# Kernel optimization log

Measured on AMD Instinct MI355X. Metric: run time of the kernel, lower is better.

## Reference

```python
import jax, jax.numpy as jnp
import numpy as np

N = 50000      # nodes
E = 800000     # edges (before self loops)
IN_DIM = 128
HID = 16
HEADS = 8
OUT_DIM = 40
NEG_SLOPE = 0.2


def setup_inputs() -> dict:
    key = jax.random.key(0)
    ks = jax.random.split(key, 10)
    x = jax.random.normal(ks[0], (N, IN_DIM), jnp.float32)
    edge_index = jax.random.randint(ks[1], (2, E), 0, N, dtype=jnp.int32)
    # layer 1: GATConv(IN_DIM, HID, heads=HEADS, concat=True)
    W1 = jax.random.normal(ks[2], (IN_DIM, HEADS * HID), jnp.float32) / np.sqrt(IN_DIM).astype(np.float32)
    att_src1 = jax.random.normal(ks[3], (HEADS, HID), jnp.float32) * 0.1
    att_dst1 = jax.random.normal(ks[4], (HEADS, HID), jnp.float32) * 0.1
    bias1 = jnp.zeros((HEADS * HID,), jnp.float32)
    # layer 2: GATConv(HEADS*HID, OUT_DIM, heads=1, concat=False)
    W2 = jax.random.normal(ks[5], (HEADS * HID, OUT_DIM), jnp.float32) / np.sqrt(HEADS * HID).astype(np.float32)
    att_src2 = jax.random.normal(ks[6], (1, OUT_DIM), jnp.float32) * 0.1
    att_dst2 = jax.random.normal(ks[7], (1, OUT_DIM), jnp.float32) * 0.1
    bias2 = jnp.zeros((OUT_DIM,), jnp.float32)
    return {"x": x, "W1": W1, "att_src1": att_src1, "att_dst1": att_dst1, "bias1": bias1,
            "W2": W2, "att_src2": att_src2, "att_dst2": att_dst2, "bias2": bias2,
            "edge_index": edge_index}


def gat_conv(x, src, dst, W, att_src, att_dst, bias, heads, dim, concat, num_nodes):
    # h: [N, H, D]
    h = (x @ W).reshape(num_nodes, heads, dim)
    a_src = jnp.sum(h * att_src, axis=-1)  # [N, H]
    a_dst = jnp.sum(h * att_dst, axis=-1)  # [N, H]
    e = a_src[src] + a_dst[dst]            # [E', H]
    e = jnp.where(e > 0, e, NEG_SLOPE * e)  # leaky_relu
    # segment softmax over edges sharing the same target node
    m = jax.ops.segment_max(e, dst, num_segments=num_nodes)  # [N, H]
    e = jnp.exp(e - m[dst])
    s = jax.ops.segment_sum(e, dst, num_segments=num_nodes)  # [N, H]
    alpha = e / (s[dst] + 1e-16)            # [E', H]
    msg = h[src] * alpha[:, :, None]        # [E', H, D]
    out = jax.ops.segment_sum(msg, dst, num_segments=num_nodes)  # [N, H, D]
    if concat:
        out = out.reshape(num_nodes, heads * dim)
    else:
        out = out.mean(axis=1)
    return out + bias


def reference(x, W1, att_src1, att_dst1, bias1, W2, att_src2, att_dst2, bias2, edge_index):
    # add self loops (PyG GATConv default)
    loop = jnp.arange(N, dtype=edge_index.dtype)
    src = jnp.concatenate([edge_index[0], loop])
    dst = jnp.concatenate([edge_index[1], loop])
    # eval mode: dropout (p=0.6) is identity
    h = gat_conv(x, src, dst, W1, att_src1, att_dst1, bias1, HEADS, HID, True, N)
    h = jax.nn.elu(h)
    out = gat_conv(h, src, dst, W2, att_src2, att_dst2, bias2, 1, OUT_DIM, False, N)
    return jax.nn.log_softmax(out, axis=1)
```

## Files before the change

### kernel.cpp

```cpp
#include <hip/hip_runtime.h>
#include <math.h>

#define IN_DIM 128
#define HEADS 8
#define HID 16
#define OUT_DIM 40
#define NEG 0.2f
#define NSLICE 8

typedef short bf16x8 __attribute__((ext_vector_type(8)));
typedef float f32x4 __attribute__((ext_vector_type(4)));

__device__ __forceinline__ unsigned short f32_to_bf16_rne(float v) {
  unsigned u = __float_as_uint(v);
  return (unsigned short)((u + 0x7FFFu + ((u >> 16) & 1u)) >> 16);
}


__global__ void hist_k(const int* __restrict__ ei, int E0, int N, int snode,
                       int* __restrict__ deg) {
  int b = blockIdx.x;
  int slice = b & (NSLICE - 1);
  int e = (b >> 3) * 256 + threadIdx.x;
  int EP = E0 + N;
  if (e >= EP) return;
  int d = (e < E0) ? ei[E0 + e] : (e - E0);
  if (d / snode == slice) atomicAdd(&deg[d], 1);
}

__global__ __launch_bounds__(1024) void scanA_k(const int* __restrict__ deg, int* __restrict__ rp,
                                                int* __restrict__ bsum, int n) {
  __shared__ int wsum[16];
  int tid = threadIdx.x;
  int i = blockIdx.x * 1024 + tid;
  int lane = tid & 63, w = tid >> 6;
  int v = (i < n) ? deg[i] : 0;
  int x = v;
  #pragma unroll
  for (int off = 1; off < 64; off <<= 1) {
    int y = __shfl_up(x, off);
    if (lane >= off) x += y;
  }
  if (lane == 63) wsum[w] = x;
  __syncthreads();
  if (tid < 16) {
    int s = wsum[tid];
    #pragma unroll
    for (int off = 1; off < 16; off <<= 1) {
      int y = __shfl_up(s, off);
      if (tid >= off) s += y;
    }
    wsum[tid] = s;
  }
  __syncthreads();
  int woff = (w == 0) ? 0 : wsum[w - 1];
  if (i < n) rp[i] = woff + x - v;
  if (tid == 0) bsum[blockIdx.x] = wsum[15];
}

__global__ __launch_bounds__(1024) void scanB_k(int* __restrict__ bsum, int nb,
                                                int* __restrict__ rp, int n) {
  __shared__ int wsum[16];
  int tid = threadIdx.x;
  int lane = tid & 63, w = tid >> 6;
  int v = (tid < nb) ? bsum[tid] : 0;
  int x = v;
  #pragma unroll
  for (int off = 1; off < 64; off <<= 1) {
    int y = __shfl_up(x, off);
    if (lane >= off) x += y;
  }
  if (lane == 63) wsum[w] = x;
  __syncthreads();
  if (tid < 16) {
    int s = wsum[tid];
    #pragma unroll
    for (int off = 1; off < 16; off <<= 1) {
      int y = __shfl_up(s, off);
      if (tid >= off) s += y;
    }
    wsum[tid] = s;
  }
  __syncthreads();
  int woff = (w == 0) ? 0 : wsum[w - 1];
  if (tid < nb) bsum[tid] = woff + x - v;
  if (tid == 0) rp[n] = wsum[15];
}

__global__ __launch_bounds__(1024) void scanC_k(int* __restrict__ rp, const int* __restrict__ bsum,
                                                int* __restrict__ cnt, int n) {
  int i = blockIdx.x * 1024 + threadIdx.x;
  if (i < n) {
    int v = rp[i] + bsum[blockIdx.x];
    rp[i] = v;
    cnt[i] = v;
  }
}

__global__ void scatter_k(const int* __restrict__ ei, int E0, int N, int snode,
                          int* __restrict__ cnt, int* __restrict__ csr_src) {
  int b = blockIdx.x;
  int slice = b & (NSLICE - 1);
  int e = (b >> 3) * 256 + threadIdx.x;
  int EP = E0 + N;
  if (e >= EP) return;
  int d = (e < E0) ? ei[E0 + e] : (e - E0);
  if (d / snode != slice) return;
  int s = (e < E0) ? ei[e] : d;
  int pos = atomicAdd(&cnt[d], 1);
  csr_src[pos] = s;
}

__global__ void prep_k(const float* __restrict__ W1, const float* __restrict__ as1,
                       const float* __restrict__ ad1, const float* __restrict__ W2,
                       const float* __restrict__ as2, const float* __restrict__ ad2,
                       unsigned short* __restrict__ whi, unsigned short* __restrict__ wlo,
                       unsigned short* __restrict__ w2p, int* __restrict__ deg, int N) {
  int t = blockIdx.x * 256 + threadIdx.x;
  if (t < N) deg[t] = 0;
  if (t < 18432) {
    int j = t & 7, lane = (t >> 3) & 63, kc = (t >> 9) & 3, ct = t >> 11;
    int k = kc * 32 + (lane >> 4) * 8 + j;
    int col = lane & 15;
    float v;
    if (ct < 8) {
      v = W1[k * 128 + ct * 16 + col];
    } else {
      int h = col & 7;
      const float* att = (col < 8) ? as1 : ad1;
      float s = 0.f;
      #pragma unroll
      for (int d = 0; d < 16; ++d) s += W1[k * 128 + h * 16 + d] * att[h * 16 + d];
      v = s;
    }
    unsigned u = __float_as_uint(v);
    unsigned hi = (u + 0x7FFFu + ((u >> 16) & 1u)) >> 16;
    float rem = v - __uint_as_float(hi << 16);
    unsigned ur = __float_as_uint(rem);
    unsigned lo = (ur + 0x7FFFu + ((ur >> 16) & 1u)) >> 16;
    whi[t] = (unsigned short)hi;
    wlo[t] = (unsigned short)lo;
  } else if (t < 18432 + 6144) {
    int u2 = t - 18432;
    int j = u2 & 7, lane = (u2 >> 3) & 63, kc = (u2 >> 9) & 3, ct = u2 >> 11;
    int k = kc * 32 + (lane >> 4) * 8 + j;
    int col = ct * 16 + (lane & 15);
    float v;
    if (col < OUT_DIM) {
      v = W2[k * OUT_DIM + col];
    } else if (col < 42) {
      const float* att = (col == OUT_DIM) ? as2 : ad2;
      float s = 0.f;
      #pragma unroll 8
      for (int d = 0; d < OUT_DIM; ++d) s += W2[k * OUT_DIM + d] * att[d];
      v = s;
    } else {
      v = 0.f;
    }
    w2p[u2] = f32_to_bf16_rne(v);
  }
}

__global__ __launch_bounds__(256) void gemm1_mfma_k(
    const float* __restrict__ x, const unsigned short* __restrict__ whi,
    const unsigned short* __restrict__ wlo,
    unsigned short* __restrict__ h1, float* __restrict__ a1s, float* __restrict__ a1d, int N) {
  int w = threadIdx.x >> 6, lane = threadIdx.x & 63;
  int quad = lane >> 4, l15 = lane & 15;
  int row = blockIdx.x * 64 + w * 16 + l15;
  int rowc = (row < N) ? row : (N - 1);

  f32x4 acc[9];
  #pragma unroll
  for (int t = 0; t < 9; ++t) acc[t] = (f32x4){0.f, 0.f, 0.f, 0.f};

  const float* xr = x + (size_t)rowc * 128 + quad * 8;
  #pragma unroll
  for (int kc = 0; kc < 4; ++kc) {
    f32x4 a0 = *reinterpret_cast<const f32x4*>(xr + kc * 32);
    f32x4 a1 = *reinterpret_cast<const f32x4*>(xr + kc * 32 + 4);
    float av[8] = {a0.x, a0.y, a0.z, a0.w, a1.x, a1.y, a1.z, a1.w};
    bf16x8 ahi, alo;
    #pragma unroll
    for (int j = 0; j < 8; ++j) {
      unsigned u = __float_as_uint(av[j]);
      unsigned hi = (u + 0x7FFFu + ((u >> 16) & 1u)) >> 16;
      float rem = av[j] - __uint_as_float(hi << 16);
      unsigned ur = __float_as_uint(rem);
      unsigned lo = (ur + 0x7FFFu + ((ur >> 16) & 1u)) >> 16;
      ahi[j] = (short)hi;
      alo[j] = (short)lo;
    }
    #pragma unroll
    for (int ct = 0; ct < 9; ++ct) {
      bf16x8 bh = *reinterpret_cast<const bf16x8*>(whi + ((size_t)(ct * 4 + kc) * 64 + lane) * 8);
      bf16x8 bl = *reinterpret_cast<const bf16x8*>(wlo + ((size_t)(ct * 4 + kc) * 64 + lane) * 8);
      acc[ct] = __builtin_amdgcn_mfma_f32_16x16x32_bf16(ahi, bh, acc[ct], 0, 0, 0);
      acc[ct] = __builtin_amdgcn_mfma_f32_16x16x32_bf16(ahi, bl, acc[ct], 0, 0, 0);
      acc[ct] = __builtin_amdgcn_mfma_f32_16x16x32_bf16(alo, bh, acc[ct], 0, 0, 0);
    }
  }
  int rbase = blockIdx.x * 64 + w * 16 + quad * 4;
  #pragma unroll
  for (int reg = 0; reg < 4; ++reg) {
    int r = rbase + reg;
    if (r < N) {
      #pragma unroll
      for (int ct = 0; ct < 8; ++ct)
        h1[(size_t)r * 128 + ct * 16 + l15] = f32_to_bf16_rne(acc[ct][reg]);
      float v = acc[8][reg];
      if (l15 < 8) a1s[r * 8 + l15] = v;
      else         a1d[r * 8 + (l15 - 8)] = v;
    }
  }
}

__global__ __launch_bounds__(256) void agg1_k(
    const int* __restrict__ row_ptr, const int* __restrict__ csr_src,
    const float* __restrict__ a1s, const float* __restrict__ a1d,
    const unsigned* __restrict__ h1u, const float* __restrict__ bias1,
    unsigned* __restrict__ vrowp, int N) {
  int wid = threadIdx.x >> 6;
  int lane = threadIdx.x & 63;
  int n = blockIdx.x * 4 + wid;
  if (n >= N) return;

  int rs = row_ptr[n], re = row_ptr[n + 1];
  int h = lane >> 3;
  float adn = a1d[n * 8 + h];

  float accx = 0.f, accy = 0.f, sw = 0.f;
  int i = rs;
  for (; i + 8 <= re; i += 8) {
    int s0 = csr_src[i],     s1 = csr_src[i + 1], s2 = csr_src[i + 2], s3 = csr_src[i + 3];
    int s4 = csr_src[i + 4], s5 = csr_src[i + 5], s6 = csr_src[i + 6], s7 = csr_src[i + 7];
    float e0 = a1s[s0 * 8 + h] + adn;
    float e1 = a1s[s1 * 8 + h] + adn;
    float e2 = a1s[s2 * 8 + h] + adn;
    float e3 = a1s[s3 * 8 + h] + adn;
    float e4 = a1s[s4 * 8 + h] + adn;
    float e5 = a1s[s5 * 8 + h] + adn;
    float e6 = a1s[s6 * 8 + h] + adn;
    float e7 = a1s[s7 * 8 + h] + adn;
    unsigned u0 = h1u[(size_t)s0 * 64 + lane];
    unsigned u1 = h1u[(size_t)s1 * 64 + lane];
    unsigned u2 = h1u[(size_t)s2 * 64 + lane];
    unsigned u3 = h1u[(size_t)s3 * 64 + lane];
    unsigned u4 = h1u[(size_t)s4 * 64 + lane];
    unsigned u5 = h1u[(size_t)s5 * 64 + lane];
    unsigned u6 = h1u[(size_t)s6 * 64 + lane];
    unsigned u7 = h1u[(size_t)s7 * 64 + lane];
    e0 = fmaxf(e0, NEG * e0); e1 = fmaxf(e1, NEG * e1);
    e2 = fmaxf(e2, NEG * e2); e3 = fmaxf(e3, NEG * e3);
    e4 = fmaxf(e4, NEG * e4); e5 = fmaxf(e5, NEG * e5);
    e6 = fmaxf(e6, NEG * e6); e7 = fmaxf(e7, NEG * e7);
    float w0 = __expf(e0), w1 = __expf(e1), w2 = __expf(e2), w3 = __expf(e3);
    float w4 = __expf(e4), w5 = __expf(e5), w6 = __expf(e6), w7 = __expf(e7);
    sw += ((w0 + w1) + (w2 + w3)) + ((w4 + w5) + (w6 + w7));
    accx += w0 * __uint_as_float(u0 << 16) + w1 * __uint_as_float(u1 << 16)
          + w2 * __uint_as_float(u2 << 16) + w3 * __uint_as_float(u3 << 16)
          + w4 * __uint_as_float(u4 << 16) + w5 * __uint_as_float(u5 << 16)
          + w6 * __uint_as_float(u6 << 16) + w7 * __uint_as_float(u7 << 16);
    accy += w0 * __uint_as_float(u0 & 0xFFFF0000u) + w1 * __uint_as_float(u1 & 0xFFFF0000u)
          + w2 * __uint_as_float(u2 & 0xFFFF0000u) + w3 * __uint_as_float(u3 & 0xFFFF0000u)
          + w4 * __uint_as_float(u4 & 0xFFFF0000u) + w5 * __uint_as_float(u5 & 0xFFFF0000u)
          + w6 * __uint_as_float(u6 & 0xFFFF0000u) + w7 * __uint_as_float(u7 & 0xFFFF0000u);
  }
  for (; i + 4 <= re; i += 4) {
    int s0 = csr_src[i], s1 = csr_src[i + 1], s2 = csr_src[i + 2], s3 = csr_src[i + 3];
    float e0 = a1s[s0 * 8 + h] + adn;
    float e1 = a1s[s1 * 8 + h] + adn;
    float e2 = a1s[s2 * 8 + h] + adn;
    float e3 = a1s[s3 * 8 + h] + adn;
    unsigned u0 = h1u[(size_t)s0 * 64 + lane];
    unsigned u1 = h1u[(size_t)s1 * 64 + lane];
    unsigned u2 = h1u[(size_t)s2 * 64 + lane];
    unsigned u3 = h1u[(size_t)s3 * 64 + lane];
    e0 = fmaxf(e0, NEG * e0); e1 = fmaxf(e1, NEG * e1);
    e2 = fmaxf(e2, NEG * e2); e3 = fmaxf(e3, NEG * e3);
    float w0 = __expf(e0), w1 = __expf(e1), w2 = __expf(e2), w3 = __expf(e3);
    sw += (w0 + w1) + (w2 + w3);
    accx += w0 * __uint_as_float(u0 << 16) + w1 * __uint_as_float(u1 << 16)
          + w2 * __uint_as_float(u2 << 16) + w3 * __uint_as_float(u3 << 16);
    accy += w0 * __uint_as_float(u0 & 0xFFFF0000u) + w1 * __uint_as_float(u1 & 0xFFFF0000u)
          + w2 * __uint_as_float(u2 & 0xFFFF0000u) + w3 * __uint_as_float(u3 & 0xFFFF0000u);
  }
  for (; i < re; ++i) {
    int s = csr_src[i];
    float e = a1s[s * 8 + h] + adn;
    e = fmaxf(e, NEG * e);
    float w = __expf(e);
    unsigned u = h1u[(size_t)s * 64 + lane];
    sw += w;
    accx += w * __uint_as_float(u << 16);
    accy += w * __uint_as_float(u & 0xFFFF0000u);
  }
  float inv = 1.f / (sw + 1e-16f);
  float2 b = *reinterpret_cast<const float2*>(bias1 + 2 * lane);
  float vx = accx * inv + b.x;
  float vy = accy * inv + b.y;
  vx = (vx > 0.f) ? vx : (__expf(vx) - 1.f);
  vy = (vy > 0.f) ? vy : (__expf(vy) - 1.f);
  unsigned packed = (unsigned)f32_to_bf16_rne(vx) | ((unsigned)f32_to_bf16_rne(vy) << 16);
  vrowp[(size_t)n * 64 + lane] = packed;
}

__global__ __launch_bounds__(256) void gemm2_mfma_k(
    const unsigned short* __restrict__ vrow, const unsigned short* __restrict__ w2p,
    unsigned short* __restrict__ h2, float* __restrict__ a2s, float* __restrict__ a2d, int N) {
  int w = threadIdx.x >> 6, lane = threadIdx.x & 63;
  int quad = lane >> 4, l15 = lane & 15;
  int row = blockIdx.x * 64 + w * 16 + l15;
  int rowc = (row < N) ? row : (N - 1);

  f32x4 acc[3];
  #pragma unroll
  for (int t = 0; t < 3; ++t) acc[t] = (f32x4){0.f, 0.f, 0.f, 0.f};

  const unsigned short* vr = vrow + (size_t)rowc * 128 + quad * 8;
  #pragma unroll
  for (int kc = 0; kc < 4; ++kc) {
    bf16x8 a = *reinterpret_cast<const bf16x8*>(vr + kc * 32);
    #pragma unroll
    for (int ct = 0; ct < 3; ++ct) {
      bf16x8 bfrag = *reinterpret_cast<const bf16x8*>(w2p + ((size_t)(ct * 4 + kc) * 64 + lane) * 8);
      acc[ct] = __builtin_amdgcn_mfma_f32_16x16x32_bf16(a, bfrag, acc[ct], 0, 0, 0);
    }
  }
  int rbase = blockIdx.x * 64 + w * 16 + quad * 4;
  #pragma unroll
  for (int reg = 0; reg < 4; ++reg) {
    int r = rbase + reg;
    if (r < N) {
      #pragma unroll
      for (int ct = 0; ct < 3; ++ct) {
        int col = ct * 16 + l15;
        float v = acc[ct][reg];
        if (col < OUT_DIM)       h2[(size_t)r * 64 + col] = f32_to_bf16_rne(v);
        else if (col == OUT_DIM) a2s[r] = v;
        else if (col == 41)      a2d[r] = v;
      }
    }
  }
}

__global__ __launch_bounds__(256) void agg2_k(
    const int* __restrict__ row_ptr, const int* __restrict__ csr_src,
    const float* __restrict__ a2s, const float* __restrict__ a2d,
    const unsigned short* __restrict__ h2, const float* __restrict__ bias2,
    float* __restrict__ out, int N) {
  int wid = threadIdx.x >> 6;
  int lane = threadIdx.x & 63;
  int n = blockIdx.x * 4 + wid;
  if (n >= N) return;

  int rs = row_ptr[n], re = row_ptr[n + 1];
  float adn = a2d[n];
  bool act = lane < OUT_DIM;
  float acc = 0.f, sw = 0.f;
  int i = rs;
  for (; i + 8 <= re; i += 8) {
    int s0 = csr_src[i],     s1 = csr_src[i + 1], s2 = csr_src[i + 2], s3 = csr_src[i + 3];
    int s4 = csr_src[i + 4], s5 = csr_src[i + 5], s6 = csr_src[i + 6], s7 = csr_src[i + 7];
    float e0 = a2s[s0] + adn, e1 = a2s[s1] + adn, e2 = a2s[s2] + adn, e3 = a2s[s3] + adn;
    float e4 = a2s[s4] + adn, e5 = a2s[s5] + adn, e6 = a2s[s6] + adn, e7 = a2s[s7] + adn;
    unsigned g0 = h2[(size_t)s0 * 64 + lane];
    unsigned g1 = h2[(size_t)s1 * 64 + lane];
    unsigned g2 = h2[(size_t)s2 * 64 + lane];
    unsigned g3 = h2[(size_t)s3 * 64 + lane];
    unsigned g4 = h2[(size_t)s4 * 64 + lane];
    unsigned g5 = h2[(size_t)s5 * 64 + lane];
    unsigned g6 = h2[(size_t)s6 * 64 + lane];
    unsigned g7 = h2[(size_t)s7 * 64 + lane];
    e0 = fmaxf(e0, NEG * e0); e1 = fmaxf(e1, NEG * e1);
    e2 = fmaxf(e2, NEG * e2); e3 = fmaxf(e3, NEG * e3);
    e4 = fmaxf(e4, NEG * e4); e5 = fmaxf(e5, NEG * e5);
    e6 = fmaxf(e6, NEG * e6); e7 = fmaxf(e7, NEG * e7);
    float w0 = __expf(e0), w1 = __expf(e1), w2 = __expf(e2), w3 = __expf(e3);
    float w4 = __expf(e4), w5 = __expf(e5), w6 = __expf(e6), w7 = __expf(e7);
    sw += ((w0 + w1) + (w2 + w3)) + ((w4 + w5) + (w6 + w7));
    acc += w0 * __uint_as_float(g0 << 16) + w1 * __uint_as_float(g1 << 16)
         + w2 * __uint_as_float(g2 << 16) + w3 * __uint_as_float(g3 << 16)
         + w4 * __uint_as_float(g4 << 16) + w5 * __uint_as_float(g5 << 16)
         + w6 * __uint_as_float(g6 << 16) + w7 * __uint_as_float(g7 << 16);
  }
  for (; i + 4 <= re; i += 4) {
    int s0 = csr_src[i], s1 = csr_src[i + 1], s2 = csr_src[i + 2], s3 = csr_src[i + 3];
    float e0 = a2s[s0] + adn, e1 = a2s[s1] + adn, e2 = a2s[s2] + adn, e3 = a2s[s3] + adn;
    unsigned g0 = h2[(size_t)s0 * 64 + lane];
    unsigned g1 = h2[(size_t)s1 * 64 + lane];
    unsigned g2 = h2[(size_t)s2 * 64 + lane];
    unsigned g3 = h2[(size_t)s3 * 64 + lane];
    e0 = fmaxf(e0, NEG * e0); e1 = fmaxf(e1, NEG * e1);
    e2 = fmaxf(e2, NEG * e2); e3 = fmaxf(e3, NEG * e3);
    float w0 = __expf(e0), w1 = __expf(e1), w2 = __expf(e2), w3 = __expf(e3);
    sw += (w0 + w1) + (w2 + w3);
    acc += w0 * __uint_as_float(g0 << 16) + w1 * __uint_as_float(g1 << 16)
         + w2 * __uint_as_float(g2 << 16) + w3 * __uint_as_float(g3 << 16);
  }
  for (; i < re; ++i) {
    int s = csr_src[i];
    float e = a2s[s] + adn;
    e = fmaxf(e, NEG * e);
    float w = __expf(e);
    sw += w;
    unsigned g = h2[(size_t)s * 64 + lane];
    acc += w * __uint_as_float(g << 16);
  }
  float v = act ? (acc / (sw + 1e-16f) + bias2[lane]) : -1e30f;
  float vm = v;
  #pragma unroll
  for (int off = 32; off > 0; off >>= 1) vm = fmaxf(vm, __shfl_xor(vm, off));
  float ex = act ? __expf(v - vm) : 0.f;
  float es = ex;
  #pragma unroll
  for (int off = 32; off > 0; off >>= 1) es += __shfl_xor(es, off);
  if (act) out[(size_t)n * OUT_DIM + lane] = v - vm - __logf(es);
}


extern "C" void kernel_launch(void* const* d_in, const int* in_sizes, int n_in,
                              void* d_out, int out_size, void* d_ws, size_t ws_size,
                              hipStream_t stream) {
  const float* x   = (const float*)d_in[0];
  const float* W1  = (const float*)d_in[1];
  const float* as1 = (const float*)d_in[2];
  const float* ad1 = (const float*)d_in[3];
  const float* b1  = (const float*)d_in[4];
  const float* W2  = (const float*)d_in[5];
  const float* as2 = (const float*)d_in[6];
  const float* ad2 = (const float*)d_in[7];
  const float* b2  = (const float*)d_in[8];
  const int*   ei  = (const int*)d_in[9];
  int N  = in_sizes[0] / IN_DIM;
  int E0 = in_sizes[9] / 2;
  int EP = E0 + N;
  int snode = (N + NSLICE - 1) / NSLICE;
  float* out = (float*)d_out;

  char* ws = (char*)d_ws;
  size_t off = 0;
  auto alloc = [&](size_t bytes) {
    char* p = ws + off;
    off += (bytes + 255) & ~size_t(255);
    return p;
  };
  unsigned short* h1   = (unsigned short*)alloc((size_t)N * 128 * 2);
  float* a1s  = (float*)alloc((size_t)N * 8 * 4);
  float* a1d  = (float*)alloc((size_t)N * 8 * 4);
  unsigned*       vrow = (unsigned*)alloc((size_t)N * 64 * 4);
  unsigned short* h2   = (unsigned short*)alloc((size_t)N * 64 * 2);
  float* a2s  = (float*)alloc((size_t)N * 4);
  float* a2d  = (float*)alloc((size_t)N * 4);
  int*   deg  = (int*)alloc((size_t)N * 4);
  int*   cnt  = (int*)alloc((size_t)N * 4);
  int*   rp   = (int*)alloc((size_t)(N + 4) * 4);
  int*   bsum = (int*)alloc((size_t)1024 * 4);
  int*   csr  = (int*)alloc((size_t)EP * 4);
  unsigned short* whi = (unsigned short*)alloc((size_t)18432 * 2);
  unsigned short* wlo = (unsigned short*)alloc((size_t)18432 * 2);
  unsigned short* w2p = (unsigned short*)alloc((size_t)6144 * 2);

  int nb = (N + 1023) / 1024;
  int nchunk = (EP + 255) / 256;
  prep_k<<<(N + 255) / 256, 256, 0, stream>>>(W1, as1, ad1, W2, as2, ad2, whi, wlo, w2p, deg, N);
  hist_k<<<nchunk * NSLICE, 256, 0, stream>>>(ei, E0, N, snode, deg);
  scanA_k<<<nb, 1024, 0, stream>>>(deg, rp, bsum, N);
  scanB_k<<<1, 1024, 0, stream>>>(bsum, nb, rp, N);
  scanC_k<<<nb, 1024, 0, stream>>>(rp, bsum, cnt, N);
  scatter_k<<<nchunk * NSLICE, 256, 0, stream>>>(ei, E0, N, snode, cnt, csr);
  gemm1_mfma_k<<<(N + 63) / 64, 256, 0, stream>>>(x, whi, wlo, h1, a1s, a1d, N);
  agg1_k<<<(N + 3) / 4, 256, 0, stream>>>(rp, csr, a1s, a1d, (const unsigned*)h1, b1, vrow, N);
  gemm2_mfma_k<<<(N + 63) / 64, 256, 0, stream>>>((const unsigned short*)vrow, w2p, h2, a2s, a2d, N);
  agg2_k<<<(N + 3) / 4, 256, 0, stream>>>(rp, csr, a2s, a2d, h2, b2, out, N);
}
```

Before: 266.8 us.

## Precompute normalized per-edge attention weights in separate kernels before aggregation

Adds w1_k and w2_k kernels that compute the edge softmax weights in two passes over each node's edges, with lanes spread across edges, and write normalized weights to new per-edge buffers. The aggregation kernels then read these precomputed weights instead of gathering a_src and evaluating exp per feature lane. This removes the redundant exp work that was repeated across lanes in the aggregation loops. In exchange it adds two kernel launches, a per-edge weight array of EP*8 floats to write and read back, and recomputes the exp in the second pass.

```diff
diff --git a/kernel.cpp b/kernel.cpp
--- a/kernel.cpp
+++ b/kernel.cpp
@@ -215,9 +215,44 @@
   }
 }
 
+__global__ __launch_bounds__(256) void w1_k(
+    const int* __restrict__ rp, const int* __restrict__ csr,
+    const float* __restrict__ a1s, const float* __restrict__ a1d,
+    float* __restrict__ w1n, int N) {
+  int wid = threadIdx.x >> 6, lane = threadIdx.x & 63;
+  int n = blockIdx.x * 4 + wid;
+  if (n >= N) return;
+  int rs = rp[n], re = rp[n + 1];
+  int slot = lane >> 3, hw = lane & 7;
+  float adn = a1d[n * 8 + hw];
+  float sw = 0.f;
+  for (int i0 = rs; i0 < re; i0 += 8) {
+    int idx = i0 + slot;
+    if (idx < re) {
+      int s = csr[idx];
+      float e = a1s[s * 8 + hw] + adn;
+      e = fmaxf(e, NEG * e);
+      sw += __expf(e);
+    }
+  }
+  sw += __shfl_xor(sw, 8);
+  sw += __shfl_xor(sw, 16);
+  sw += __shfl_xor(sw, 32);
+  float inv = 1.f / (sw + 1e-16f);
+  for (int i0 = rs; i0 < re; i0 += 8) {
+    int idx = i0 + slot;
+    if (idx < re) {
+      int s = csr[idx];
+      float e = a1s[s * 8 + hw] + adn;
+      e = fmaxf(e, NEG * e);
+      w1n[(size_t)idx * 8 + hw] = __expf(e) * inv;
+    }
+  }
+}
+
 __global__ __launch_bounds__(256) void agg1_k(
     const int* __restrict__ row_ptr, const int* __restrict__ csr_src,
-    const float* __restrict__ a1s, const float* __restrict__ a1d,
+    const float* __restrict__ w1n,
     const unsigned* __restrict__ h1u, const float* __restrict__ bias1,
     unsigned* __restrict__ vrowp, int N) {
   int wid = threadIdx.x >> 6;
@@ -227,21 +262,20 @@
 
   int rs = row_ptr[n], re = row_ptr[n + 1];
   int h = lane >> 3;
-  float adn = a1d[n * 8 + h];
-
-  float accx = 0.f, accy = 0.f, sw = 0.f;
+
+  float accx = 0.f, accy = 0.f;
   int i = rs;
   for (; i + 8 <= re; i += 8) {
     int s0 = csr_src[i],     s1 = csr_src[i + 1], s2 = csr_src[i + 2], s3 = csr_src[i + 3];
     int s4 = csr_src[i + 4], s5 = csr_src[i + 5], s6 = csr_src[i + 6], s7 = csr_src[i + 7];
-    float e0 = a1s[s0 * 8 + h] + adn;
-    float e1 = a1s[s1 * 8 + h] + adn;
-    float e2 = a1s[s2 * 8 + h] + adn;
-    float e3 = a1s[s3 * 8 + h] + adn;
-    float e4 = a1s[s4 * 8 + h] + adn;
-    float e5 = a1s[s5 * 8 + h] + adn;
-    float e6 = a1s[s6 * 8 + h] + adn;
-    float e7 = a1s[s7 * 8 + h] + adn;
+    float w0 = w1n[(size_t)(i + 0) * 8 + h];
+    float w1 = w1n[(size_t)(i + 1) * 8 + h];
+    float w2 = w1n[(size_t)(i + 2) * 8 + h];
+    float w3 = w1n[(size_t)(i + 3) * 8 + h];
+    float w4 = w1n[(size_t)(i + 4) * 8 + h];
+    float w5 = w1n[(size_t)(i + 5) * 8 + h];
+    float w6 = w1n[(size_t)(i + 6) * 8 + h];
+    float w7 = w1n[(size_t)(i + 7) * 8 + h];
     unsigned u0 = h1u[(size_t)s0 * 64 + lane];
     unsigned u1 = h1u[(size_t)s1 * 64 + lane];
     unsigned u2 = h1u[(size_t)s2 * 64 + lane];
@@ -250,13 +284,6 @@
     unsigned u5 = h1u[(size_t)s5 * 64 + lane];
     unsigned u6 = h1u[(size_t)s6 * 64 + lane];
     unsigned u7 = h1u[(size_t)s7 * 64 + lane];
-    e0 = fmaxf(e0, NEG * e0); e1 = fmaxf(e1, NEG * e1);
-    e2 = fmaxf(e2, NEG * e2); e3 = fmaxf(e3, NEG * e3);
-    e4 = fmaxf(e4, NEG * e4); e5 = fmaxf(e5, NEG * e5);
-    e6 = fmaxf(e6, NEG * e6); e7 = fmaxf(e7, NEG * e7);
-    float w0 = __expf(e0), w1 = __expf(e1), w2 = __expf(e2), w3 = __expf(e3);
-    float w4 = __expf(e4), w5 = __expf(e5), w6 = __expf(e6), w7 = __expf(e7);
-    sw += ((w0 + w1) + (w2 + w3)) + ((w4 + w5) + (w6 + w7));
     accx += w0 * __uint_as_float(u0 << 16) + w1 * __uint_as_float(u1 << 16)
           + w2 * __uint_as_float(u2 << 16) + w3 * __uint_as_float(u3 << 16)
           + w4 * __uint_as_float(u4 << 16) + w5 * __uint_as_float(u5 << 16)
@@ -268,18 +295,14 @@
   }
   for (; i + 4 <= re; i += 4) {
     int s0 = csr_src[i], s1 = csr_src[i + 1], s2 = csr_src[i + 2], s3 = csr_src[i + 3];
-    float e0 = a1s[s0 * 8 + h] + adn;
-    float e1 = a1s[s1 * 8 + h] + adn;
-    float e2 = a1s[s2 * 8 + h] + adn;
-    float e3 = a1s[s3 * 8 + h] + adn;
+    float w0 = w1n[(size_t)(i + 0) * 8 + h];
+    float w1 = w1n[(size_t)(i + 1) * 8 + h];
+    float w2 = w1n[(size_t)(i + 2) * 8 + h];
+    float w3 = w1n[(size_t)(i + 3) * 8 + h];
     unsigned u0 = h1u[(size_t)s0 * 64 + lane];
     unsigned u1 = h1u[(size_t)s1 * 64 + lane];
     unsigned u2 = h1u[(size_t)s2 * 64 + lane];
     unsigned u3 = h1u[(size_t)s3 * 64 + lane];
-    e0 = fmaxf(e0, NEG * e0); e1 = fmaxf(e1, NEG * e1);
-    e2 = fmaxf(e2, NEG * e2); e3 = fmaxf(e3, NEG * e3);
-    float w0 = __expf(e0), w1 = __expf(e1), w2 = __expf(e2), w3 = __expf(e3);
-    sw += (w0 + w1) + (w2 + w3);
     accx += w0 * __uint_as_float(u0 << 16) + w1 * __uint_as_float(u1 << 16)
           + w2 * __uint_as_float(u2 << 16) + w3 * __uint_as_float(u3 << 16);
     accy += w0 * __uint_as_float(u0 & 0xFFFF0000u) + w1 * __uint_as_float(u1 & 0xFFFF0000u)
@@ -287,18 +310,14 @@
   }
   for (; i < re; ++i) {
     int s = csr_src[i];
-    float e = a1s[s * 8 + h] + adn;
-    e = fmaxf(e, NEG * e);
-    float w = __expf(e);
+    float w = w1n[(size_t)i * 8 + h];
     unsigned u = h1u[(size_t)s * 64 + lane];
-    sw += w;
     accx += w * __uint_as_float(u << 16);
     accy += w * __uint_as_float(u & 0xFFFF0000u);
   }
-  float inv = 1.f / (sw + 1e-16f);
   float2 b = *reinterpret_cast<const float2*>(bias1 + 2 * lane);
-  float vx = accx * inv + b.x;
-  float vy = accy * inv + b.y;
+  float vx = accx + b.x;
+  float vy = accy + b.y;
   vx = (vx > 0.f) ? vx : (__expf(vx) - 1.f);
   vy = (vy > 0.f) ? vy : (__expf(vy) - 1.f);
   unsigned packed = (unsigned)f32_to_bf16_rne(vx) | ((unsigned)f32_to_bf16_rne(vy) << 16);
@@ -344,9 +363,36 @@
   }
 }
 
+__global__ __launch_bounds__(256) void w2_k(
+    const int* __restrict__ rp, const int* __restrict__ csr,
+    const float* __restrict__ a2s, const float* __restrict__ a2d,
+    float* __restrict__ w2n, int N) {
+  int wid = threadIdx.x >> 6, lane = threadIdx.x & 63;
+  int n = blockIdx.x * 4 + wid;
+  if (n >= N) return;
+  int rs = rp[n], re = rp[n + 1];
+  float adn = a2d[n];
+  float sw = 0.f;
+  for (int i = rs + lane; i < re; i += 64) {
+    int s = csr[i];
+    float e = a2s[s] + adn;
+    e = fmaxf(e, NEG * e);
+    sw += __expf(e);
+  }
+  #pragma unroll
+  for (int off = 32; off > 0; off >>= 1) sw += __shfl_xor(sw, off);
+  float inv = 1.f / (sw + 1e-16f);
+  for (int i = rs + lane; i < re; i += 64) {
+    int s = csr[i];
+    float e = a2s[s] + adn;
+    e = fmaxf(e, NEG * e);
+    w2n[i] = __expf(e) * inv;
+  }
+}
+
 __global__ __launch_bounds__(256) void agg2_k(
     const int* __restrict__ row_ptr, const int* __restrict__ csr_src,
-    const float* __restrict__ a2s, const float* __restrict__ a2d,
+    const float* __restrict__ w2n,
     const unsigned short* __restrict__ h2, const float* __restrict__ bias2,
     float* __restrict__ out, int N) {
   int wid = threadIdx.x >> 6;
@@ -355,15 +401,14 @@
   if (n >= N) return;
 
   int rs = row_ptr[n], re = row_ptr[n + 1];
-  float adn = a2d[n];
   bool act = lane < OUT_DIM;
-  float acc = 0.f, sw = 0.f;
+  float acc = 0.f;
   int i = rs;
   for (; i + 8 <= re; i += 8) {
     int s0 = csr_src[i],     s1 = csr_src[i + 1], s2 = csr_src[i + 2], s3 = csr_src[i + 3];
     int s4 = csr_src[i + 4], s5 = csr_src[i + 5], s6 = csr_src[i + 6], s7 = csr_src[i + 7];
-    float e0 = a2s[s0] + adn, e1 = a2s[s1] + adn, e2 = a2s[s2] + adn, e3 = a2s[s3] + adn;
-    float e4 = a2s[s4] + adn, e5 = a2s[s5] + adn, e6 = a2s[s6] + adn, e7 = a2s[s7] + adn;
+    float w0 = w2n[i],     w1 = w2n[i + 1], w2 = w2n[i + 2], w3 = w2n[i + 3];
+    float w4 = w2n[i + 4], w5 = w2n[i + 5], w6 = w2n[i + 6], w7 = w2n[i + 7];
     unsigned g0 = h2[(size_t)s0 * 64 + lane];
     unsigned g1 = h2[(size_t)s1 * 64 + lane];
     unsigned g2 = h2[(size_t)s2 * 64 + lane];
@@ -372,13 +417,6 @@
     unsigned g5 = h2[(size_t)s5 * 64 + lane];
     unsigned g6 = h2[(size_t)s6 * 64 + lane];
     unsigned g7 = h2[(size_t)s7 * 64 + lane];
-    e0 = fmaxf(e0, NEG * e0); e1 = fmaxf(e1, NEG * e1);
-    e2 = fmaxf(e2, NEG * e2); e3 = fmaxf(e3, NEG * e3);
-    e4 = fmaxf(e4, NEG * e4); e5 = fmaxf(e5, NEG * e5);
-    e6 = fmaxf(e6, NEG * e6); e7 = fmaxf(e7, NEG * e7);
-    float w0 = __expf(e0), w1 = __expf(e1), w2 = __expf(e2), w3 = __expf(e3);
-    float w4 = __expf(e4), w5 = __expf(e5), w6 = __expf(e6), w7 = __expf(e7);
-    sw += ((w0 + w1) + (w2 + w3)) + ((w4 + w5) + (w6 + w7));
     acc += w0 * __uint_as_float(g0 << 16) + w1 * __uint_as_float(g1 << 16)
          + w2 * __uint_as_float(g2 << 16) + w3 * __uint_as_float(g3 << 16)
          + w4 * __uint_as_float(g4 << 16) + w5 * __uint_as_float(g5 << 16)
@@ -386,28 +424,21 @@
   }
   for (; i + 4 <= re; i += 4) {
     int s0 = csr_src[i], s1 = csr_src[i + 1], s2 = csr_src[i + 2], s3 = csr_src[i + 3];
-    float e0 = a2s[s0] + adn, e1 = a2s[s1] + adn, e2 = a2s[s2] + adn, e3 = a2s[s3] + adn;
+    float w0 = w2n[i], w1 = w2n[i + 1], w2 = w2n[i + 2], w3 = w2n[i + 3];
     unsigned g0 = h2[(size_t)s0 * 64 + lane];
     unsigned g1 = h2[(size_t)s1 * 64 + lane];
     unsigned g2 = h2[(size_t)s2 * 64 + lane];
     unsigned g3 = h2[(size_t)s3 * 64 + lane];
-    e0 = fmaxf(e0, NEG * e0); e1 = fmaxf(e1, NEG * e1);
-    e2 = fmaxf(e2, NEG * e2); e3 = fmaxf(e3, NEG * e3);
-    float w0 = __expf(e0), w1 = __expf(e1), w2 = __expf(e2), w3 = __expf(e3);
-    sw += (w0 + w1) + (w2 + w3);
     acc += w0 * __uint_as_float(g0 << 16) + w1 * __uint_as_float(g1 << 16)
          + w2 * __uint_as_float(g2 << 16) + w3 * __uint_as_float(g3 << 16);
   }
   for (; i < re; ++i) {
     int s = csr_src[i];
-    float e = a2s[s] + adn;
-    e = fmaxf(e, NEG * e);
-    float w = __expf(e);
-    sw += w;
+    float w = w2n[i];
     unsigned g = h2[(size_t)s * 64 + lane];
     acc += w * __uint_as_float(g << 16);
   }
-  float v = act ? (acc / (sw + 1e-16f) + bias2[lane]) : -1e30f;
+  float v = act ? (acc + bias2[lane]) : -1e30f;
   float vm = v;
   #pragma unroll
   for (int off = 32; off > 0; off >>= 1) vm = fmaxf(vm, __shfl_xor(vm, off));
@@ -452,6 +483,8 @@
   unsigned short* h2   = (unsigned short*)alloc((size_t)N * 64 * 2);
   float* a2s  = (float*)alloc((size_t)N * 4);
   float* a2d  = (float*)alloc((size_t)N * 4);
+  float* w1n  = (float*)alloc((size_t)EP * 8 * 4);
+  float* w2n  = (float*)alloc((size_t)EP * 4);
   int*   deg  = (int*)alloc((size_t)N * 4);
   int*   cnt  = (int*)alloc((size_t)N * 4);
   int*   rp   = (int*)alloc((size_t)(N + 4) * 4);
@@ -470,7 +503,9 @@
   scanC_k<<<nb, 1024, 0, stream>>>(rp, bsum, cnt, N);
   scatter_k<<<nchunk * NSLICE, 256, 0, stream>>>(ei, E0, N, snode, cnt, csr);
   gemm1_mfma_k<<<(N + 63) / 64, 256, 0, stream>>>(x, whi, wlo, h1, a1s, a1d, N);
-  agg1_k<<<(N + 3) / 4, 256, 0, stream>>>(rp, csr, a1s, a1d, (const unsigned*)h1, b1, vrow, N);
+  w1_k<<<(N + 3) / 4, 256, 0, stream>>>(rp, csr, a1s, a1d, w1n, N);
+  agg1_k<<<(N + 3) / 4, 256, 0, stream>>>(rp, csr, w1n, (const unsigned*)h1, b1, vrow, N);
   gemm2_mfma_k<<<(N + 63) / 64, 256, 0, stream>>>((const unsigned short*)vrow, w2p, h2, a2s, a2d, N);
-  agg2_k<<<(N + 3) / 4, 256, 0, stream>>>(rp, csr, a2s, a2d, h2, b2, out, N);
-}
+  w2_k<<<(N + 3) / 4, 256, 0, stream>>>(rp, csr, a2s, a2d, w2n, N);
+  agg2_k<<<(N + 3) / 4, 256, 0, stream>>>(rp, csr, w2n, h2, b2, out, N);
+}
```

Result: slower. 300.0 us (+12.4%).

## Precompute per-edge attention weights in LDS before gathering features in aggregation

Applied to the files above, without the earlier changes.

Both aggregation kernels become two-phase. First, lanes cooperatively compute the edge scores, exp weights and softmax sum in parallel and stage the weights and source indices in shared memory, up to 128 edges per node. The gather loop then reads those staged values with vector LDS loads instead of recomputing exp and re-reading the attention scalars in every lane. Edges past 128 fall back to the old path, and the extra LDS use may reduce occupancy.

```diff
diff --git a/kernel.cpp b/kernel.cpp
--- a/kernel.cpp
+++ b/kernel.cpp
@@ -223,79 +223,84 @@
   int wid = threadIdx.x >> 6;
   int lane = threadIdx.x & 63;
   int n = blockIdx.x * 4 + wid;
+
+  __shared__ __align__(16) float wls_s[4][8 * 132];
+  __shared__ __align__(16) int   srcs_s[4][128];
+
   if (n >= N) return;
+  float* wls  = wls_s[wid];
+  int*   srcs = srcs_s[wid];
 
   int rs = row_ptr[n], re = row_ptr[n + 1];
+  int deg = re - rs;
+  int slot = lane >> 3, hw = lane & 7;
+  float adn = a1d[n * 8 + hw];
+
+  float sw = 0.f;
+  for (int i0 = 0; i0 < deg; i0 += 8) {
+    int idx = i0 + slot;
+    bool val = idx < deg;
+    int s = csr_src[rs + (val ? idx : deg - 1)];
+    float e = a1s[s * 8 + hw] + adn;
+    e = fmaxf(e, NEG * e);
+    float w = val ? __expf(e) : 0.f;
+    sw += w;
+    if (val && idx < 128) {
+      wls[hw * 132 + idx] = w;
+      if (hw == 0) srcs[idx] = s;
+    }
+  }
+  sw += __shfl_xor(sw, 8);
+  sw += __shfl_xor(sw, 16);
+  sw += __shfl_xor(sw, 32);
   int h = lane >> 3;
-  float adn = a1d[n * 8 + h];
-
-  float accx = 0.f, accy = 0.f, sw = 0.f;
-  int i = rs;
-  for (; i + 8 <= re; i += 8) {
-    int s0 = csr_src[i],     s1 = csr_src[i + 1], s2 = csr_src[i + 2], s3 = csr_src[i + 3];
-    int s4 = csr_src[i + 4], s5 = csr_src[i + 5], s6 = csr_src[i + 6], s7 = csr_src[i + 7];
-    float e0 = a1s[s0 * 8 + h] + adn;
-    float e1 = a1s[s1 * 8 + h] + adn;
-    float e2 = a1s[s2 * 8 + h] + adn;
-    float e3 = a1s[s3 * 8 + h] + adn;
-    float e4 = a1s[s4 * 8 + h] + adn;
-    float e5 = a1s[s5 * 8 + h] + adn;
-    float e6 = a1s[s6 * 8 + h] + adn;
-    float e7 = a1s[s7 * 8 + h] + adn;
-    unsigned u0 = h1u[(size_t)s0 * 64 + lane];
-    unsigned u1 = h1u[(size_t)s1 * 64 + lane];
-    unsigned u2 = h1u[(size_t)s2 * 64 + lane];
-    unsigned u3 = h1u[(size_t)s3 * 64 + lane];
-    unsigned u4 = h1u[(size_t)s4 * 64 + lane];
-    unsigned u5 = h1u[(size_t)s5 * 64 + lane];
-    unsigned u6 = h1u[(size_t)s6 * 64 + lane];
-    unsigned u7 = h1u[(size_t)s7 * 64 + lane];
-    e0 = fmaxf(e0, NEG * e0); e1 = fmaxf(e1, NEG * e1);
-    e2 = fmaxf(e2, NEG * e2); e3 = fmaxf(e3, NEG * e3);
-    e4 = fmaxf(e4, NEG * e4); e5 = fmaxf(e5, NEG * e5);
-    e6 = fmaxf(e6, NEG * e6); e7 = fmaxf(e7, NEG * e7);
-    float w0 = __expf(e0), w1 = __expf(e1), w2 = __expf(e2), w3 = __expf(e3);
-    float w4 = __expf(e4), w5 = __expf(e5), w6 = __expf(e6), w7 = __expf(e7);
-    sw += ((w0 + w1) + (w2 + w3)) + ((w4 + w5) + (w6 + w7));
-    accx += w0 * __uint_as_float(u0 << 16) + w1 * __uint_as_float(u1 << 16)
-          + w2 * __uint_as_float(u2 << 16) + w3 * __uint_as_float(u3 << 16)
-          + w4 * __uint_as_float(u4 << 16) + w5 * __uint_as_float(u5 << 16)
-          + w6 * __uint_as_float(u6 << 16) + w7 * __uint_as_float(u7 << 16);
-    accy += w0 * __uint_as_float(u0 & 0xFFFF0000u) + w1 * __uint_as_float(u1 & 0xFFFF0000u)
-          + w2 * __uint_as_float(u2 & 0xFFFF0000u) + w3 * __uint_as_float(u3 & 0xFFFF0000u)
-          + w4 * __uint_as_float(u4 & 0xFFFF0000u) + w5 * __uint_as_float(u5 & 0xFFFF0000u)
-          + w6 * __uint_as_float(u6 & 0xFFFF0000u) + w7 * __uint_as_float(u7 & 0xFFFF0000u);
-  }
-  for (; i + 4 <= re; i += 4) {
-    int s0 = csr_src[i], s1 = csr_src[i + 1], s2 = csr_src[i + 2], s3 = csr_src[i + 3];
-    float e0 = a1s[s0 * 8 + h] + adn;
-    float e1 = a1s[s1 * 8 + h] + adn;
-    float e2 = a1s[s2 * 8 + h] + adn;
-    float e3 = a1s[s3 * 8 + h] + adn;
-    unsigned u0 = h1u[(size_t)s0 * 64 + lane];
-    unsigned u1 = h1u[(size_t)s1 * 64 + lane];
-    unsigned u2 = h1u[(size_t)s2 * 64 + lane];
-    unsigned u3 = h1u[(size_t)s3 * 64 + lane];
-    e0 = fmaxf(e0, NEG * e0); e1 = fmaxf(e1, NEG * e1);
-    e2 = fmaxf(e2, NEG * e2); e3 = fmaxf(e3, NEG * e3);
-    float w0 = __expf(e0), w1 = __expf(e1), w2 = __expf(e2), w3 = __expf(e3);
-    sw += (w0 + w1) + (w2 + w3);
-    accx += w0 * __uint_as_float(u0 << 16) + w1 * __uint_as_float(u1 << 16)
-          + w2 * __uint_as_float(u2 << 16) + w3 * __uint_as_float(u3 << 16);
-    accy += w0 * __uint_as_float(u0 & 0xFFFF0000u) + w1 * __uint_as_float(u1 & 0xFFFF0000u)
-          + w2 * __uint_as_float(u2 & 0xFFFF0000u) + w3 * __uint_as_float(u3 & 0xFFFF0000u);
-  }
-  for (; i < re; ++i) {
-    int s = csr_src[i];
-    float e = a1s[s * 8 + h] + adn;
-    e = fmaxf(e, NEG * e);
-    float w = __expf(e);
+  float inv = __shfl(1.f / (sw + 1e-16f), h);
+
+  float accx = 0.f, accy = 0.f;
+  int lim = (deg < 128) ? deg : 128;
+  const float* wh = wls + h * 132;
+  int i = 0;
+  for (; i + 8 <= lim; i += 8) {
+    int4 sa = *reinterpret_cast<const int4*>(srcs + i);
+    int4 sb = *reinterpret_cast<const int4*>(srcs + i + 4);
+    float4 wa = *reinterpret_cast<const float4*>(wh + i);
+    float4 wb = *reinterpret_cast<const float4*>(wh + i + 4);
+    unsigned u0 = h1u[(size_t)sa.x * 64 + lane];
+    unsigned u1 = h1u[(size_t)sa.y * 64 + lane];
+    unsigned u2 = h1u[(size_t)sa.z * 64 + lane];
+    unsigned u3 = h1u[(size_t)sa.w * 64 + lane];
+    unsigned u4 = h1u[(size_t)sb.x * 64 + lane];
+    unsigned u5 = h1u[(size_t)sb.y * 64 + lane];
+    unsigned u6 = h1u[(size_t)sb.z * 64 + lane];
+    unsigned u7 = h1u[(size_t)sb.w * 64 + lane];
+    accx += wa.x * __uint_as_float(u0 << 16) + wa.y * __uint_as_float(u1 << 16)
+          + wa.z * __uint_as_float(u2 << 16) + wa.w * __uint_as_float(u3 << 16)
+          + wb.x * __uint_as_float(u4 << 16) + wb.y * __uint_as_float(u5 << 16)
+          + wb.z * __uint_as_float(u6 << 16) + wb.w * __uint_as_float(u7 << 16);
+    accy += wa.x * __uint_as_float(u0 & 0xFFFF0000u) + wa.y * __uint_as_float(u1 & 0xFFFF0000u)
+          + wa.z * __uint_as_float(u2 & 0xFFFF0000u) + wa.w * __uint_as_float(u3 & 0xFFFF0000u)
+          + wb.x * __uint_as_float(u4 & 0xFFFF0000u) + wb.y * __uint_as_float(u5 & 0xFFFF0000u)
+          + wb.z * __uint_as_float(u6 & 0xFFFF0000u) + wb.w * __uint_as_float(u7 & 0xFFFF0000u);
+  }
+  for (; i < lim; ++i) {
+    int s = srcs[i];
+    float w = wh[i];
     unsigned u = h1u[(size_t)s * 64 + lane];
-    sw += w;
     accx += w * __uint_as_float(u << 16);
     accy += w * __uint_as_float(u & 0xFFFF0000u);
   }
-  float inv = 1.f / (sw + 1e-16f);
+  if (deg > 128) {
+    float adn2 = a1d[n * 8 + h];
+    for (int j2 = 128; j2 < deg; ++j2) {
+      int s = csr_src[rs + j2];
+      float e = a1s[s * 8 + h] + adn2;
+      e = fmaxf(e, NEG * e);
+      float w = __expf(e);
+      unsigned u = h1u[(size_t)s * 64 + lane];
+      accx += w * __uint_as_float(u << 16);
+      accy += w * __uint_as_float(u & 0xFFFF0000u);
+    }
+  }
   float2 b = *reinterpret_cast<const float2*>(bias1 + 2 * lane);
   float vx = accx * inv + b.x;
   float vy = accy * inv + b.y;
@@ -352,62 +357,72 @@
   int wid = threadIdx.x >> 6;
   int lane = threadIdx.x & 63;
   int n = blockIdx.x * 4 + wid;
+
+  __shared__ __align__(16) float wls_s[4][128];
+  __shared__ __align__(16) int   srcs_s[4][128];
+
   if (n >= N) return;
+  float* wls  = wls_s[wid];
+  int*   srcs = srcs_s[wid];
 
   int rs = row_ptr[n], re = row_ptr[n + 1];
+  int deg = re - rs;
   float adn = a2d[n];
-  bool act = lane < OUT_DIM;
-  float acc = 0.f, sw = 0.f;
-  int i = rs;
-  for (; i + 8 <= re; i += 8) {
-    int s0 = csr_src[i],     s1 = csr_src[i + 1], s2 = csr_src[i + 2], s3 = csr_src[i + 3];
-    int s4 = csr_src[i + 4], s5 = csr_src[i + 5], s6 = csr_src[i + 6], s7 = csr_src[i + 7];
-    float e0 = a2s[s0] + adn, e1 = a2s[s1] + adn, e2 = a2s[s2] + adn, e3 = a2s[s3] + adn;
-    float e4 = a2s[s4] + adn, e5 = a2s[s5] + adn, e6 = a2s[s6] + adn, e7 = a2s[s7] + adn;
-    unsigned g0 = h2[(size_t)s0 * 64 + lane];
-    unsigned g1 = h2[(size_t)s1 * 64 + lane];
-    unsigned g2 = h2[(size_t)s2 * 64 + lane];
-    unsigned g3 = h2[(size_t)s3 * 64 + lane];
-    unsigned g4 = h2[(size_t)s4 * 64 + lane];
-    unsigned g5 = h2[(size_t)s5 * 64 + lane];
-    unsigned g6 = h2[(size_t)s6 * 64 + lane];
-    unsigned g7 = h2[(size_t)s7 * 64 + lane];
-    e0 = fmaxf(e0, NEG * e0); e1 = fmaxf(e1, NEG * e1);
-    e2 = fmaxf(e2, NEG * e2); e3 = fmaxf(e3, NEG * e3);
-    e4 = fmaxf(e4, NEG * e4); e5 = fmaxf(e5, NEG * e5);
-    e6 = fmaxf(e6, NEG * e6); e7 = fmaxf(e7, NEG * e7);
-    float w0 = __expf(e0), w1 = __expf(e1), w2 = __expf(e2), w3 = __expf(e3);
-    float w4 = __expf(e4), w5 = __expf(e5), w6 = __expf(e6), w7 = __expf(e7);
-    sw += ((w0 + w1) + (w2 + w3)) + ((w4 + w5) + (w6 + w7));
-    acc += w0 * __uint_as_float(g0 << 16) + w1 * __uint_as_float(g1 << 16)
-         + w2 * __uint_as_float(g2 << 16) + w3 * __uint_as_float(g3 << 16)
-         + w4 * __uint_as_float(g4 << 16) + w5 * __uint_as_float(g5 << 16)
-         + w6 * __uint_as_float(g6 << 16) + w7 * __uint_as_float(g7 << 16);
-  }
-  for (; i + 4 <= re; i += 4) {
-    int s0 = csr_src[i], s1 = csr_src[i + 1], s2 = csr_src[i + 2], s3 = csr_src[i + 3];
-    float e0 = a2s[s0] + adn, e1 = a2s[s1] + adn, e2 = a2s[s2] + adn, e3 = a2s[s3] + adn;
-    unsigned g0 = h2[(size_t)s0 * 64 + lane];
-    unsigned g1 = h2[(size_t)s1 * 64 + lane];
-    unsigned g2 = h2[(size_t)s2 * 64 + lane];
-    unsigned g3 = h2[(size_t)s3 * 64 + lane];
-    e0 = fmaxf(e0, NEG * e0); e1 = fmaxf(e1, NEG * e1);
-    e2 = fmaxf(e2, NEG * e2); e3 = fmaxf(e3, NEG * e3);
-    float w0 = __expf(e0), w1 = __expf(e1), w2 = __expf(e2), w3 = __expf(e3);
-    sw += (w0 + w1) + (w2 + w3);
-    acc += w0 * __uint_as_float(g0 << 16) + w1 * __uint_as_float(g1 << 16)
-         + w2 * __uint_as_float(g2 << 16) + w3 * __uint_as_float(g3 << 16);
-  }
-  for (; i < re; ++i) {
-    int s = csr_src[i];
+
+  float sw = 0.f;
+  for (int i0 = 0; i0 < deg; i0 += 64) {
+    int idx = i0 + lane;
+    bool val = idx < deg;
+    int s = csr_src[rs + (val ? idx : deg - 1)];
     float e = a2s[s] + adn;
     e = fmaxf(e, NEG * e);
-    float w = __expf(e);
+    float w = val ? __expf(e) : 0.f;
     sw += w;
+    if (val && idx < 128) { wls[idx] = w; srcs[idx] = s; }
+  }
+  #pragma unroll
+  for (int off = 32; off > 0; off >>= 1) sw += __shfl_xor(sw, off);
+  float inv = 1.f / (sw + 1e-16f);
+
+  bool act = lane < OUT_DIM;
+  float acc = 0.f;
+  int lim = (deg < 128) ? deg : 128;
+  int i = 0;
+  for (; i + 8 <= lim; i += 8) {
+    int4 sa = *reinterpret_cast<const int4*>(srcs + i);
+    int4 sb = *reinterpret_cast<const int4*>(srcs + i + 4);
+    float4 wa = *reinterpret_cast<const float4*>(wls + i);
+    float4 wb = *reinterpret_cast<const float4*>(wls + i + 4);
+    unsigned g0 = h2[(size_t)sa.x * 64 + lane];
+    unsigned g1 = h2[(size_t)sa.y * 64 + lane];
+    unsigned g2 = h2[(size_t)sa.z * 64 + lane];
+    unsigned g3 = h2[(size_t)sa.w * 64 + lane];
+    unsigned g4 = h2[(size_t)sb.x * 64 + lane];
+    unsigned g5 = h2[(size_t)sb.y * 64 + lane];
+    unsigned g6 = h2[(size_t)sb.z * 64 + lane];
+    unsigned g7 = h2[(size_t)sb.w * 64 + lane];
+    acc += wa.x * __uint_as_float(g0 << 16) + wa.y * __uint_as_float(g1 << 16)
+         + wa.z * __uint_as_float(g2 << 16) + wa.w * __uint_as_float(g3 << 16)
+         + wb.x * __uint_as_float(g4 << 16) + wb.y * __uint_as_float(g5 << 16)
+         + wb.z * __uint_as_float(g6 << 16) + wb.w * __uint_as_float(g7 << 16);
+  }
+  for (; i < lim; ++i) {
+    int s = srcs[i];
+    float w = wls[i];
     unsigned g = h2[(size_t)s * 64 + lane];
     acc += w * __uint_as_float(g << 16);
   }
-  float v = act ? (acc / (sw + 1e-16f) + bias2[lane]) : -1e30f;
+  if (deg > 128) {
+    for (int j2 = 128; j2 < deg; ++j2) {
+      int s = csr_src[rs + j2];
+      float e = a2s[s] + adn;
+      e = fmaxf(e, NEG * e);
+      float w = __expf(e);
+      unsigned g = h2[(size_t)s * 64 + lane];
+      acc += w * __uint_as_float(g << 16);
+    }
+  }
+  float v = act ? (acc * inv + bias2[lane]) : -1e30f;
   float vm = v;
   #pragma unroll
   for (int off = 32; off > 0; off >>= 1) vm = fmaxf(vm, __shfl_xor(vm, off));
```

New measurement: 270.0 us. No clear change (+1.2%).
